# Performance work log

Measured on AMD Instinct MI355X. Metric: run time of the kernel, lower is better.

## Reference

```python
import jax, jax.numpy as jnp
import numpy as np

B, M, N = 8, 2048, 8192
K = 8            # knn neighbors
HID = 128        # hidden_dim
IN_DIM = 6
OUT_W = 2        # out_width (deconv kernel=stride=2 on length-1 seed)


def setup_inputs() -> dict:
    key = jax.random.key(0)
    ks = jax.random.split(key, 12)
    s = 0.1  # weight scale
    return {
        "partial": jax.random.normal(ks[0], (B, M, 3), jnp.float32),
        "predicted": jax.random.normal(ks[1], (B, N, 3), jnp.float32),
        # seed_fc: Linear(6,128) -> ReLU -> Linear(128,128)
        "W1": jax.random.normal(ks[2], (HID, IN_DIM), jnp.float32) * s,
        "b1": jax.random.normal(ks[3], (HID,), jnp.float32) * s,
        "W2": jax.random.normal(ks[4], (HID, HID), jnp.float32) * s,
        "b2": jax.random.normal(ks[5], (HID,), jnp.float32) * s,
        # ConvTranspose1d(HID, HID, kernel=2, stride=2): weight [in, out, kT]
        "Wd": jax.random.normal(ks[6], (HID, HID, OUT_W), jnp.float32) * s,
        "bd": jax.random.normal(ks[7], (HID,), jnp.float32) * s,
        # Conv1d(HID, 3, kernel=1): weight [3, HID, 1]
        "Wc": jax.random.normal(ks[8], (3, HID, 1), jnp.float32) * s,
        "bc": jax.random.normal(ks[9], (3,), jnp.float32) * s,
    }


def _forward(partial, predicted, W1, b1, W2, b2, Wd, bd, Wc, bc):
    Bb, Nn, _ = predicted.shape
    # squared pairwise distances [B,N,M] (same ordering as torch.cdist p=2)
    d2 = (jnp.sum(predicted ** 2, -1)[:, :, None]
          - 2.0 * jnp.einsum('bnd,bmd->bnm', predicted, partial)
          + jnp.sum(partial ** 2, -1)[:, None, :])
    _, idx = jax.lax.top_k(-d2, K)                       # [B,N,K] nearest
    neigh = jax.vmap(lambda p, i: p[i])(partial, idx)    # [B,N,K,3] gather
    neigh_mean = neigh.mean(axis=2)                      # [B,N,3]
    combined = jnp.concatenate([predicted, neigh_mean], -1).reshape(Bb * Nn, IN_DIM)
    # seed MLP
    h = jax.nn.relu(combined @ W1.T + b1)
    seed = h @ W2.T + b2                                 # [BN,HID]
    # ConvTranspose1d on length-1 input: out[:, o, t] = sum_i seed[:, i] * Wd[i, o, t]
    ht = jax.nn.relu(jnp.einsum('bi,iot->bot', seed, Wd) + bd[None, :, None])  # [BN,HID,2]
    out = jnp.einsum('bit,ci->bct', ht, Wc[:, :, 0]) + bc[None, :, None]       # [BN,3,2]
    out4 = jnp.transpose(out, (0, 2, 1)).reshape(Bb, Nn, OUT_W, 3)
    child = predicted[:, :, None, :] + out4              # parent + offsets
    return child.reshape(Bb, Nn * OUT_W, 3)


def reference(partial, predicted, W1, b1, W2, b2, Wd, bd, Wc, bc):
    return _forward(partial, predicted, W1, b1, W2, b2, Wd, bd, Wc, bc)
```

## Files before the change

kernel.cpp:

```cpp
#include <hip/hip_runtime.h>
#include <hip/hip_bf16.h>
#include <math.h>

#define TPB 256
constexpr int Bb = 8, Mm = 2048, Nn = 8192, HID = 128;
constexpr int KNNB = Bb * 128;
constexpr int PREPB = 128;

typedef __attribute__((ext_vector_type(8))) short short8;
typedef __attribute__((ext_vector_type(4))) float f32x4;

__device__ __forceinline__ int vzero() { int v; asm("v_mov_b32 %0, 0" : "=v"(v)); return v; }
__device__ __forceinline__ float4 ldg4(const float* __restrict__ p, int idx4, int vz) {
  return ((const float4*)p)[idx4 + vz];
}
__device__ __forceinline__ unsigned short f2b(float x) {
  __hip_bfloat16 h = __float2bfloat16(x);
  return *reinterpret_cast<unsigned short*>(&h);
}

__device__ __forceinline__ void mergeTop8(float a[8], const float b[8]) {
  float w[8];
  #pragma unroll
  for (int i = 0; i < 8; ++i) w[i] = fmaxf(a[i], b[7 - i]);
  #pragma unroll
  for (int i = 0; i < 4; ++i) {
    float lo = fminf(w[i], w[i + 4]); w[i + 4] = fmaxf(w[i], w[i + 4]); w[i] = lo;
  }
  #pragma unroll
  for (int g = 0; g < 8; g += 4)
    #pragma unroll
    for (int i = 0; i < 2; ++i) {
      float lo = fminf(w[g + i], w[g + i + 2]);
      w[g + i + 2] = fmaxf(w[g + i], w[g + i + 2]); w[g + i] = lo;
    }
  #pragma unroll
  for (int i = 0; i < 8; i += 2) {
    float lo = fminf(w[i], w[i + 1]); w[i + 1] = fmaxf(w[i], w[i + 1]); w[i] = lo;
  }
  #pragma unroll
  for (int i = 0; i < 8; ++i) a[i] = w[i];
}
__device__ __forceinline__ float t8of(const float a[8], const float b[8]) {
  float t = fmaxf(a[0], b[7]);
  #pragma unroll
  for (int i = 1; i < 8; ++i) t = fminf(t, fmaxf(a[i], b[7 - i]));
  return t;
}

#define INSERT8(L, u)                                                          \
  {                                                                            \
    L[0] = __builtin_amdgcn_fmed3f(u, L[0], L[1]);                             \
    L[1] = __builtin_amdgcn_fmed3f(u, L[1], L[2]);                             \
    L[2] = __builtin_amdgcn_fmed3f(u, L[2], L[3]);                             \
    L[3] = __builtin_amdgcn_fmed3f(u, L[3], L[4]);                             \
    L[4] = __builtin_amdgcn_fmed3f(u, L[4], L[5]);                             \
    L[5] = __builtin_amdgcn_fmed3f(u, L[5], L[6]);                             \
    L[6] = __builtin_amdgcn_fmed3f(u, L[6], L[7]);                             \
    L[7] = fmaxf(L[7], u);                                                     \
  }

__global__ __launch_bounds__(TPB, 4) void knn_prep_kernel(
    const float* __restrict__ partial, const float* __restrict__ predicted,
    const float* __restrict__ W2, const float* __restrict__ b2,
    const float* __restrict__ Wd, const float* __restrict__ bd,
    unsigned short* __restrict__ Bpack, float* __restrict__ Cf,
    float* __restrict__ outp) {
  __shared__ float4 pts[Mm];
  const int tid = threadIdx.x;

  if (blockIdx.x >= KNNB) {
    int idx = (blockIdx.x - KNNB) * TPB + tid;
    int f = idx >> 9, r = idx & 511, lane = r >> 3, j = r & 7;
    int chunk = f >> 4, ks = (f >> 2) & 3, n = f & 3;
    int k   = ks * 32 + (lane >> 4) * 8 + j;
    int col = chunk * 64 + n * 16 + (lane & 15);
    float acc = 0.f;
    for (int i = 0; i < HID; ++i)
      acc = fmaf(W2[i * HID + k], Wd[i * 256 + col], acc);
    Bpack[idx] = f2b(acc);
    if (idx < 256) {
      float c = bd[idx >> 1];
      for (int i = 0; i < HID; ++i) c = fmaf(b2[i], Wd[i * 256 + idx], c);
      Cf[idx] = c;
    }
    return;
  }

  const int b  = blockIdx.x >> 7;
  const int qt = blockIdx.x & 127;
  const float* pb = partial + (size_t)b * Mm * 3;
  for (int i = tid; i < Mm; i += TPB) {
    float x = pb[3 * i], y = pb[3 * i + 1], z = pb[3 * i + 2];
    pts[i] = make_float4(x, y, z, -0.5f * fmaf(x, x, fmaf(y, y, z * z)));
  }
  __syncthreads();

  const int lane = tid & 63, w = tid >> 6;
  const int s = lane & 15, g = lane >> 4;
  const int qbase = qt * 64 + w * 16 + g * 4;
  const float4* qp = (const float4*)(predicted + ((size_t)b * Nn + qbase) * 3);
  const float4 qa = qp[0], qb4 = qp[1], qc = qp[2];
  const float q0x = qa.x,  q0y = qa.y,  q0z = qa.z;
  const float q1x = qa.w,  q1y = qb4.x, q1z = qb4.y;
  const float q2x = qb4.z, q2y = qb4.w, q2z = qc.x;
  const float q3x = qc.y,  q3y = qc.z,  q3z = qc.w;

  float l0[8], l1[8], l2[8], l3[8];
  #pragma unroll
  for (int i = 0; i < 8; ++i) { l0[i] = -INFINITY; l1[i] = -INFINITY;
                                l2[i] = -INFINITY; l3[i] = -INFINITY; }
  #pragma unroll 4
  for (int mm = 0; mm < 128; ++mm) {
    float4 p = pts[s + 16 * mm];
    float u0 = fmaf(q0x, p.x, fmaf(q0y, p.y, fmaf(q0z, p.z, p.w)));
    float u1 = fmaf(q1x, p.x, fmaf(q1y, p.y, fmaf(q1z, p.z, p.w)));
    float u2 = fmaf(q2x, p.x, fmaf(q2y, p.y, fmaf(q2z, p.z, p.w)));
    float u3 = fmaf(q3x, p.x, fmaf(q3y, p.y, fmaf(q3z, p.z, p.w)));
    INSERT8(l0, u0); INSERT8(l1, u1); INSERT8(l2, u2); INSERT8(l3, u3);
  }

  #pragma unroll
  for (int dd = 0; dd < 3; ++dd) {
    const int d = 1 << dd;
    float ob[8];
    #pragma unroll
    for (int i = 0; i < 8; ++i) ob[i] = __shfl_xor(l0[i], d);
    mergeTop8(l0, ob);
    #pragma unroll
    for (int i = 0; i < 8; ++i) ob[i] = __shfl_xor(l1[i], d);
    mergeTop8(l1, ob);
    #pragma unroll
    for (int i = 0; i < 8; ++i) ob[i] = __shfl_xor(l2[i], d);
    mergeTop8(l2, ob);
    #pragma unroll
    for (int i = 0; i < 8; ++i) ob[i] = __shfl_xor(l3[i], d);
    mergeTop8(l3, ob);
  }
  float t80, t81, t82, t83;
  {
    float ob[8];
    #pragma unroll
    for (int i = 0; i < 8; ++i) ob[i] = __shfl_xor(l0[i], 8);
    t80 = t8of(l0, ob);
    #pragma unroll
    for (int i = 0; i < 8; ++i) ob[i] = __shfl_xor(l1[i], 8);
    t81 = t8of(l1, ob);
    #pragma unroll
    for (int i = 0; i < 8; ++i) ob[i] = __shfl_xor(l2[i], 8);
    t82 = t8of(l2, ob);
    #pragma unroll
    for (int i = 0; i < 8; ++i) ob[i] = __shfl_xor(l3[i], 8);
    t83 = t8of(l3, ob);
  }

  float a0x = 0.f, a0y = 0.f, a0z = 0.f, c0 = 0.f;
  float a1x = 0.f, a1y = 0.f, a1z = 0.f, c1 = 0.f;
  float a2x = 0.f, a2y = 0.f, a2z = 0.f, c2 = 0.f;
  float a3x = 0.f, a3y = 0.f, a3z = 0.f, c3 = 0.f;
  #pragma unroll 4
  for (int mm = 0; mm < 128; ++mm) {
    float4 p = pts[s + 16 * mm];
    float u0 = fmaf(q0x, p.x, fmaf(q0y, p.y, fmaf(q0z, p.z, p.w)));
    float u1 = fmaf(q1x, p.x, fmaf(q1y, p.y, fmaf(q1z, p.z, p.w)));
    float u2 = fmaf(q2x, p.x, fmaf(q2y, p.y, fmaf(q2z, p.z, p.w)));
    float u3 = fmaf(q3x, p.x, fmaf(q3y, p.y, fmaf(q3z, p.z, p.w)));
    float m0 = (u0 >= t80) ? 1.f : 0.f;
    float m1 = (u1 >= t81) ? 1.f : 0.f;
    float m2 = (u2 >= t82) ? 1.f : 0.f;
    float m3 = (u3 >= t83) ? 1.f : 0.f;
    a0x = fmaf(m0, p.x, a0x); a0y = fmaf(m0, p.y, a0y); a0z = fmaf(m0, p.z, a0z); c0 += m0;
    a1x = fmaf(m1, p.x, a1x); a1y = fmaf(m1, p.y, a1y); a1z = fmaf(m1, p.z, a1z); c1 += m1;
    a2x = fmaf(m2, p.x, a2x); a2y = fmaf(m2, p.y, a2y); a2z = fmaf(m2, p.z, a2z); c2 += m2;
    a3x = fmaf(m3, p.x, a3x); a3y = fmaf(m3, p.y, a3y); a3z = fmaf(m3, p.z, a3z); c3 += m3;
  }
  #pragma unroll
  for (int dd = 0; dd < 4; ++dd) {
    const int d = 1 << dd;
    a0x += __shfl_xor(a0x, d); a0y += __shfl_xor(a0y, d); a0z += __shfl_xor(a0z, d); c0 += __shfl_xor(c0, d);
    a1x += __shfl_xor(a1x, d); a1y += __shfl_xor(a1y, d); a1z += __shfl_xor(a1z, d); c1 += __shfl_xor(c1, d);
    a2x += __shfl_xor(a2x, d); a2y += __shfl_xor(a2y, d); a2z += __shfl_xor(a2z, d); c2 += __shfl_xor(c2, d);
    a3x += __shfl_xor(a3x, d); a3y += __shfl_xor(a3y, d); a3z += __shfl_xor(a3z, d); c3 += __shfl_xor(c3, d);
  }

  #pragma unroll
  for (int k = 0; k < 4; ++k) {
    if (s == k) {
      float qx = (k == 0) ? q0x : (k == 1) ? q1x : (k == 2) ? q2x : q3x;
      float qy = (k == 0) ? q0y : (k == 1) ? q1y : (k == 2) ? q2y : q3y;
      float qz = (k == 0) ? q0z : (k == 1) ? q1z : (k == 2) ? q2z : q3z;
      float t8 = (k == 0) ? t80 : (k == 1) ? t81 : (k == 2) ? t82 : t83;
      float sx = (k == 0) ? a0x : (k == 1) ? a1x : (k == 2) ? a2x : a3x;
      float sy = (k == 0) ? a0y : (k == 1) ? a1y : (k == 2) ? a2y : a3y;
      float sz = (k == 0) ? a0z : (k == 1) ? a1z : (k == 2) ? a2z : a3z;
      float cn = (k == 0) ? c0  : (k == 1) ? c1  : (k == 2) ? c2  : c3;
      if (cn != 8.0f) {
        sx = sy = sz = 0.f; float cw = 0.f;
        for (int m = 0; m < Mm; ++m) {
          float4 p = pts[m];
          float u = fmaf(qx, p.x, fmaf(qy, p.y, fmaf(qz, p.z, p.w)));
          if (u > t8) { sx += p.x; sy += p.y; sz += p.z; cw += 1.f; }
        }
        int need = 8 - (int)cw, got = 0;
        for (int m = 0; m < Mm && got < need; ++m) {
          float4 p = pts[m];
          float u = fmaf(qx, p.x, fmaf(qy, p.y, fmaf(qz, p.z, p.w)));
          if (u == t8) { sx += p.x; sy += p.y; sz += p.z; ++got; }
        }
      }
      float2* co = (float2*)(outp + ((size_t)b * Nn + qbase + k) * 6);
      co[0] = make_float2(qx, qy);
      co[1] = make_float2(qz, sx * 0.125f);
      co[2] = make_float2(sy * 0.125f, sz * 0.125f);
    }
  }
}

__global__ __launch_bounds__(TPB) void prep2_kernel(const float* __restrict__ W2,
    const float* __restrict__ b2, const float* __restrict__ Wd,
    const float* __restrict__ bd, unsigned short* __restrict__ Bpack,
    float* __restrict__ Cf) {
  int idx = blockIdx.x * TPB + threadIdx.x;
  int f = idx >> 9, r = idx & 511, lane = r >> 3, j = r & 7;
  int chunk = f >> 4, ks = (f >> 2) & 3, n = f & 3;
  int k   = ks * 32 + (lane >> 4) * 8 + j;
  int col = chunk * 64 + n * 16 + (lane & 15);
  float acc = 0.f;
  for (int i = 0; i < HID; ++i)
    acc = fmaf(W2[i * HID + k], Wd[i * 256 + col], acc);
  Bpack[idx] = f2b(acc);
  if (idx < 256) {
    float c = bd[idx >> 1];
    for (int i = 0; i < HID; ++i) c = fmaf(b2[i], Wd[i * 256 + idx], c);
    Cf[idx] = c;
  }
}

__global__ __launch_bounds__(TPB) void mlp_mfma(const float* __restrict__ W1,
    const float* __restrict__ b1, const unsigned short* __restrict__ Bpack,
    const float* __restrict__ Cf, const float* __restrict__ Wc,
    const float* __restrict__ bc, float* __restrict__ outp) {
  extern __shared__ char Alds[];
  const int tid = threadIdx.x;
  const int row0 = blockIdx.x * TPB;
  const int vz = vzero();

  {
    const float* rp = outp + (size_t)(row0 + tid) * 6;
    float2 r0 = *(const float2*)rp, r1 = *(const float2*)(rp + 2),
           r2 = *(const float2*)(rp + 4);
    const float c0 = r0.x, c1 = r0.y, c2 = r1.x, c3 = r1.y, c4 = r2.x, c5 = r2.y;
    float4 h4[32];
    #pragma unroll
    for (int j4 = 0; j4 < 32; ++j4) {
      float4 bb = ((const float4*)b1)[j4];
      float4 w0 = ldg4(W1, j4 * 6 + 0, vz), w1 = ldg4(W1, j4 * 6 + 1, vz),
             w2 = ldg4(W1, j4 * 6 + 2, vz), w3 = ldg4(W1, j4 * 6 + 3, vz),
             w4 = ldg4(W1, j4 * 6 + 4, vz), w5 = ldg4(W1, j4 * 6 + 5, vz);
      float a0 = bb.x, a1 = bb.y, a2 = bb.z, a3 = bb.w;
      a0 = fmaf(c0, w0.x, a0); a0 = fmaf(c1, w0.y, a0); a0 = fmaf(c2, w0.z, a0);
      a0 = fmaf(c3, w0.w, a0); a0 = fmaf(c4, w1.x, a0); a0 = fmaf(c5, w1.y, a0);
      a1 = fmaf(c0, w1.z, a1); a1 = fmaf(c1, w1.w, a1); a1 = fmaf(c2, w2.x, a1);
      a1 = fmaf(c3, w2.y, a1); a1 = fmaf(c4, w2.z, a1); a1 = fmaf(c5, w2.w, a1);
      a2 = fmaf(c0, w3.x, a2); a2 = fmaf(c1, w3.y, a2); a2 = fmaf(c2, w3.z, a2);
      a2 = fmaf(c3, w3.w, a2); a2 = fmaf(c4, w4.x, a2); a2 = fmaf(c5, w4.y, a2);
      a3 = fmaf(c0, w4.z, a3); a3 = fmaf(c1, w4.w, a3); a3 = fmaf(c2, w5.x, a3);
      a3 = fmaf(c3, w5.y, a3); a3 = fmaf(c4, w5.z, a3); a3 = fmaf(c5, w5.w, a3);
      h4[j4] = make_float4(fmaxf(a0, 0.f), fmaxf(a1, 0.f), fmaxf(a2, 0.f), fmaxf(a3, 0.f));
    }
    #pragma unroll
    for (int c = 0; c < 16; ++c) {
      float4 lo = h4[c * 2], hi = h4[c * 2 + 1];
      union { unsigned short us[8]; uint4 v; } pk;
      pk.us[0] = f2b(lo.x); pk.us[1] = f2b(lo.y); pk.us[2] = f2b(lo.z); pk.us[3] = f2b(lo.w);
      pk.us[4] = f2b(hi.x); pk.us[5] = f2b(hi.y); pk.us[6] = f2b(hi.z); pk.us[7] = f2b(hi.w);
      int byte = tid * 256 + ((c * 16) ^ ((tid & 7) << 4));
      *(uint4*)(Alds + byte) = pk.v;
    }
  }
  __syncthreads();

  const int lane = tid & 63, wid = tid >> 6;
  const int g = lane >> 4, cidx = lane & 15;
  float ac[4][4][3] = {};

  for (int chunk = 0; chunk < 4; ++chunk) {
    f32x4 acc[4][4];
    #pragma unroll
    for (int n = 0; n < 4; ++n) {
      float cfv = Cf[chunk * 64 + n * 16 + cidx];
      #pragma unroll
      for (int m = 0; m < 4; ++m) acc[m][n] = (f32x4){cfv, cfv, cfv, cfv};
    }
    #pragma unroll
    for (int ks = 0; ks < 4; ++ks) {
      short8 af[4];
      #pragma unroll
      for (int m = 0; m < 4; ++m) {
        int r = wid * 64 + m * 16 + cidx;
        int byte = r * 256 + ((ks * 64 + g * 16) ^ ((r & 7) << 4));
        af[m] = *(const short8*)(Alds + byte);
      }
      short8 bf[4];
      #pragma unroll
      for (int n = 0; n < 4; ++n)
        bf[n] = *(const short8*)((const char*)Bpack +
                 (((chunk * 4 + ks) * 4 + n) * 1024) + lane * 16);
      #pragma unroll
      for (int m = 0; m < 4; ++m)
        #pragma unroll
        for (int n = 0; n < 4; ++n)
          acc[m][n] = __builtin_amdgcn_mfma_f32_16x16x32_bf16(af[m], bf[n], acc[m][n], 0, 0, 0);
    }
    #pragma unroll
    for (int n = 0; n < 4; ++n) {
      int ot = chunk * 64 + n * 16 + cidx;
      int o = ot >> 1;
      float wc0 = Wc[o], wc1 = Wc[HID + o], wc2 = Wc[2 * HID + o];
      #pragma unroll
      for (int m = 0; m < 4; ++m) {
        #pragma unroll
        for (int i = 0; i < 4; ++i) {
          float v = fmaxf(acc[m][n][i], 0.f);
          ac[m][i][0] = fmaf(v, wc0, ac[m][i][0]);
          ac[m][i][1] = fmaf(v, wc1, ac[m][i][1]);
          ac[m][i][2] = fmaf(v, wc2, ac[m][i][2]);
        }
      }
    }
  }

  const float bc0 = bc[0], bc1 = bc[1], bc2 = bc[2];
  #pragma unroll
  for (int m = 0; m < 4; ++m) {
    #pragma unroll
    for (int i = 0; i < 4; ++i) {
      float s0 = ac[m][i][0], s1 = ac[m][i][1], s2 = ac[m][i][2];
      s0 += __shfl_xor(s0, 2); s0 += __shfl_xor(s0, 4); s0 += __shfl_xor(s0, 8);
      s1 += __shfl_xor(s1, 2); s1 += __shfl_xor(s1, 4); s1 += __shfl_xor(s1, 8);
      s2 += __shfl_xor(s2, 2); s2 += __shfl_xor(s2, 4); s2 += __shfl_xor(s2, 8);
      float o0 = __shfl_xor(s0, 1), o1 = __shfl_xor(s1, 1), o2 = __shfl_xor(s2, 1);
      const bool odd = lane & 1;
      float t00 = odd ? o0 : s0, t01 = odd ? o1 : s1, t02 = odd ? o2 : s2;
      float t10 = odd ? s0 : o0, t11 = odd ? s1 : o1, t12 = odd ? s2 : o2;
      if (cidx == m * 4 + i) {
        int row = row0 + wid * 64 + m * 16 + g * 4 + i;
        float* rp = outp + (size_t)row * 6;
        float px = rp[0], py = rp[1], pz = rp[2];
        rp[0] = px + t00 + bc0; rp[1] = py + t01 + bc1; rp[2] = pz + t02 + bc2;
        rp[3] = px + t10 + bc0; rp[4] = py + t11 + bc1; rp[5] = pz + t12 + bc2;
      }
    }
  }
}

__global__ __launch_bounds__(TPB) void mlp_fallback(
    const float* __restrict__ W1, const float* __restrict__ b1,
    const float* __restrict__ W2, const float* __restrict__ b2,
    const float* __restrict__ Wd, const float* __restrict__ bd,
    const float* __restrict__ Wc, const float* __restrict__ bc,
    float* __restrict__ outp) {
  const int row = blockIdx.x * TPB + threadIdx.x;
  float2* rp = (float2*)(outp + (size_t)row * 6);
  float2 r0 = rp[0], r1 = rp[1], r2 = rp[2];
  float cc[6] = {r0.x, r0.y, r1.x, r1.y, r2.x, r2.y};
  float h[HID];
  for (int j = 0; j < HID; ++j) {
    float a = b1[j];
    for (int c = 0; c < 6; ++c) a = fmaf(cc[c], W1[j * 6 + c], a);
    h[j] = fmaxf(a, 0.f);
  }
  float sd[HID];
  for (int i = 0; i < HID; ++i) {
    float a = b2[i];
    for (int j = 0; j < HID; ++j) a = fmaf(h[j], W2[i * HID + j], a);
    sd[i] = a;
  }
  float ov[3][2] = {};
  for (int oc = 0; oc < HID; ++oc)
    for (int t = 0; t < 2; ++t) {
      float a = bd[oc];
      for (int i = 0; i < HID; ++i) a = fmaf(sd[i], Wd[i * 256 + oc * 2 + t], a);
      a = fmaxf(a, 0.f);
      for (int c = 0; c < 3; ++c) ov[c][t] = fmaf(a, Wc[c * HID + oc], ov[c][t]);
    }
  rp[0] = make_float2(cc[0] + ov[0][0] + bc[0], cc[1] + ov[1][0] + bc[1]);
  rp[1] = make_float2(cc[2] + ov[2][0] + bc[2], cc[0] + ov[0][1] + bc[0]);
  rp[2] = make_float2(cc[1] + ov[1][1] + bc[1], cc[2] + ov[2][1] + bc[2]);
}

extern "C" void kernel_launch(void* const* d_in, const int* in_sizes, int n_in,
                              void* d_out, int out_size, void* d_ws, size_t ws_size,
                              hipStream_t stream) {
  const float* partial   = (const float*)d_in[0];
  const float* predicted = (const float*)d_in[1];
  const float* W1 = (const float*)d_in[2];
  const float* b1 = (const float*)d_in[3];
  const float* W2 = (const float*)d_in[4];
  const float* b2 = (const float*)d_in[5];
  const float* Wd = (const float*)d_in[6];
  const float* bd = (const float*)d_in[7];
  const float* Wc = (const float*)d_in[8];
  const float* bc = (const float*)d_in[9];
  float* outp = (float*)d_out;

  unsigned short* Bpack = (unsigned short*)d_ws;
  float* Cf = (float*)((char*)d_ws + 65536);
  const bool fits = ws_size >= (size_t)66560;

  if (fits) {
    hipLaunchKernelGGL(knn_prep_kernel, dim3(KNNB + PREPB), dim3(TPB), 0, stream,
                       partial, predicted, W2, b2, Wd, bd, Bpack, Cf, outp);
    hipLaunchKernelGGL(mlp_mfma, dim3((Bb * Nn) / TPB), dim3(TPB), 65536, stream,
                       W1, b1, Bpack, Cf, Wc, bc, outp);
  } else {
    hipLaunchKernelGGL(knn_prep_kernel, dim3(KNNB), dim3(TPB), 0, stream,
                       partial, predicted, W2, b2, Wd, bd,
                       (unsigned short*)nullptr, (float*)nullptr, outp);
    hipLaunchKernelGGL(mlp_fallback, dim3((Bb * Nn) / TPB), dim3(TPB), 0, stream,
                       W1, b1, W2, b2, Wd, bd, Wc, bc, outp);
  }
}
```

Before: 89.22 us.

## Fuse kNN and MLP into one cooperative kernel with grid sync

Merges the kNN/prep kernel and the MFMA MLP kernel into a single cooperative launch. Each block keeps its queries' combined features in registers, computes the packed weight product in the first blocks, grid-syncs, then runs the MLP on the same rows. This removes the second launch and the round trip of intermediate features through global memory. The cost is a grid-wide barrier and the requirement that all 1024 blocks be co-resident, with a two-kernel fallback if the cooperative launch fails.

```diff
diff --git a/kernel.cpp b/kernel.cpp
--- a/kernel.cpp
+++ b/kernel.cpp
@@ -1,6 +1,9 @@
 #include <hip/hip_runtime.h>
 #include <hip/hip_bf16.h>
+#include <hip/hip_cooperative_groups.h>
 #include <math.h>
+
+namespace cg = cooperative_groups;
 
 #define TPB 256
 constexpr int Bb = 8, Mm = 2048, Nn = 8192, HID = 128;
@@ -60,35 +63,10 @@
     L[7] = fmaxf(L[7], u);                                                     \
   }
 
-__global__ __launch_bounds__(TPB, 4) void knn_prep_kernel(
-    const float* __restrict__ partial, const float* __restrict__ predicted,
-    const float* __restrict__ W2, const float* __restrict__ b2,
-    const float* __restrict__ Wd, const float* __restrict__ bd,
-    unsigned short* __restrict__ Bpack, float* __restrict__ Cf,
-    float* __restrict__ outp) {
-  __shared__ float4 pts[Mm];
-  const int tid = threadIdx.x;
-
-  if (blockIdx.x >= KNNB) {
-    int idx = (blockIdx.x - KNNB) * TPB + tid;
-    int f = idx >> 9, r = idx & 511, lane = r >> 3, j = r & 7;
-    int chunk = f >> 4, ks = (f >> 2) & 3, n = f & 3;
-    int k   = ks * 32 + (lane >> 4) * 8 + j;
-    int col = chunk * 64 + n * 16 + (lane & 15);
-    float acc = 0.f;
-    for (int i = 0; i < HID; ++i)
-      acc = fmaf(W2[i * HID + k], Wd[i * 256 + col], acc);
-    Bpack[idx] = f2b(acc);
-    if (idx < 256) {
-      float c = bd[idx >> 1];
-      for (int i = 0; i < HID; ++i) c = fmaf(b2[i], Wd[i * 256 + idx], c);
-      Cf[idx] = c;
-    }
-    return;
-  }
-
-  const int b  = blockIdx.x >> 7;
-  const int qt = blockIdx.x & 127;
+__device__ __forceinline__ void knn_phase(const float* __restrict__ partial,
+                                          const float* __restrict__ predicted,
+                                          float4* pts, int b, int qt, int tid,
+                                          float cq[6], float* wrOut) {
   const float* pb = partial + (size_t)b * Mm * 3;
   for (int i = tid; i < Mm; i += TPB) {
     float x = pb[3 * i], y = pb[3 * i + 1], z = pb[3 * i + 2];
@@ -208,19 +186,22 @@
           if (u == t8) { sx += p.x; sy += p.y; sz += p.z; ++got; }
         }
       }
-      float2* co = (float2*)(outp + ((size_t)b * Nn + qbase + k) * 6);
-      co[0] = make_float2(qx, qy);
-      co[1] = make_float2(qz, sx * 0.125f);
-      co[2] = make_float2(sy * 0.125f, sz * 0.125f);
-    }
-  }
-}
-
-__global__ __launch_bounds__(TPB) void prep2_kernel(const float* __restrict__ W2,
+      cq[0] = qx; cq[1] = qy; cq[2] = qz;
+      cq[3] = sx * 0.125f; cq[4] = sy * 0.125f; cq[5] = sz * 0.125f;
+      if (wrOut) {
+        float2* co = (float2*)(wrOut + ((size_t)b * Nn + qbase + k) * 6);
+        co[0] = make_float2(cq[0], cq[1]);
+        co[1] = make_float2(cq[2], cq[3]);
+        co[2] = make_float2(cq[4], cq[5]);
+      }
+    }
+  }
+}
+
+__device__ __forceinline__ void prep_work(int idx, const float* __restrict__ W2,
     const float* __restrict__ b2, const float* __restrict__ Wd,
     const float* __restrict__ bd, unsigned short* __restrict__ Bpack,
     float* __restrict__ Cf) {
-  int idx = blockIdx.x * TPB + threadIdx.x;
   int f = idx >> 9, r = idx & 511, lane = r >> 3, j = r & 7;
   int chunk = f >> 4, ks = (f >> 2) & 3, n = f & 3;
   int k   = ks * 32 + (lane >> 4) * 8 + j;
@@ -236,6 +217,136 @@
   }
 }
 
+__global__ __launch_bounds__(TPB, 4) void fused_kernel(
+    const float* __restrict__ partial, const float* __restrict__ predicted,
+    const float* __restrict__ W1, const float* __restrict__ b1,
+    const float* __restrict__ W2, const float* __restrict__ b2,
+    const float* __restrict__ Wd, const float* __restrict__ bd,
+    const float* __restrict__ Wc, const float* __restrict__ bc,
+    unsigned short* __restrict__ Bpack, float* __restrict__ Cf,
+    float* __restrict__ outp) {
+  __shared__ float4 smem[Mm];
+  const int tid = threadIdx.x, bid = blockIdx.x;
+  const int b = bid >> 7, qt = bid & 127;
+  const int lane = tid & 63, w = tid >> 6;
+
+  float cq[6] = {0.f, 0.f, 0.f, 0.f, 0.f, 0.f};
+  knn_phase(partial, predicted, smem, b, qt, tid, cq, nullptr);
+  if (bid < PREPB)
+    prep_work(bid * TPB + tid, W2, b2, Wd, bd, Bpack, Cf);
+
+  cg::this_grid().sync();
+
+  char* Alds = (char*)smem;
+  {
+    const int rr = lane >> 2, q4 = lane & 3;
+    const int srcl = (rr & 3) + ((rr >> 2) << 4);
+    const float c0 = __shfl(cq[0], srcl), c1 = __shfl(cq[1], srcl),
+                c2 = __shfl(cq[2], srcl), c3 = __shfl(cq[3], srcl),
+                c4 = __shfl(cq[4], srcl), c5 = __shfl(cq[5], srcl);
+    const int rowA = w * 16 + rr;
+    const int j0 = q4 * 32;
+    const float4* W1f = (const float4*)W1;
+    float hbuf[32];
+    #pragma unroll
+    for (int jj = 0; jj < 16; ++jj) {
+      float4 v0 = W1f[q4 * 48 + jj * 3 + 0];
+      float4 v1 = W1f[q4 * 48 + jj * 3 + 1];
+      float4 v2 = W1f[q4 * 48 + jj * 3 + 2];
+      int j = j0 + jj * 2;
+      float a = b1[j], e = b1[j + 1];
+      a = fmaf(c0, v0.x, a); a = fmaf(c1, v0.y, a); a = fmaf(c2, v0.z, a);
+      a = fmaf(c3, v0.w, a); a = fmaf(c4, v1.x, a); a = fmaf(c5, v1.y, a);
+      e = fmaf(c0, v1.z, e); e = fmaf(c1, v1.w, e); e = fmaf(c2, v2.x, e);
+      e = fmaf(c3, v2.y, e); e = fmaf(c4, v2.z, e); e = fmaf(c5, v2.w, e);
+      hbuf[jj * 2] = fmaxf(a, 0.f); hbuf[jj * 2 + 1] = fmaxf(e, 0.f);
+    }
+    #pragma unroll
+    for (int cc = 0; cc < 4; ++cc) {
+      union { unsigned short us[8]; uint4 v; } pk;
+      #pragma unroll
+      for (int e2 = 0; e2 < 8; ++e2) pk.us[e2] = f2b(hbuf[cc * 8 + e2]);
+      int cglob = q4 * 4 + cc;
+      int byte = rowA * 256 + ((cglob * 16) ^ ((rowA & 7) << 4));
+      *(uint4*)(Alds + byte) = pk.v;
+    }
+  }
+  __syncthreads();
+
+  const int g2 = lane >> 4, cidx = lane & 15;
+  const int rA = w * 16 + cidx;
+  float ac[4][3] = {};
+  for (int chunk = 0; chunk < 4; ++chunk) {
+    f32x4 acc[4];
+    #pragma unroll
+    for (int n = 0; n < 4; ++n) {
+      float cfv = Cf[chunk * 64 + n * 16 + cidx];
+      acc[n] = (f32x4){cfv, cfv, cfv, cfv};
+    }
+    #pragma unroll
+    for (int ks = 0; ks < 4; ++ks) {
+      short8 af = *(const short8*)(Alds + rA * 256 +
+                                   ((ks * 64 + g2 * 16) ^ ((rA & 7) << 4)));
+      #pragma unroll
+      for (int n = 0; n < 4; ++n) {
+        short8 bf = *(const short8*)((const char*)Bpack +
+                     (((chunk * 4 + ks) * 4 + n) * 1024) + lane * 16);
+        acc[n] = __builtin_amdgcn_mfma_f32_16x16x32_bf16(af, bf, acc[n], 0, 0, 0);
+      }
+    }
+    #pragma unroll
+    for (int n = 0; n < 4; ++n) {
+      int ot = chunk * 64 + n * 16 + cidx;
+      int o = ot >> 1;
+      float wc0 = Wc[o], wc1 = Wc[HID + o], wc2 = Wc[2 * HID + o];
+      #pragma unroll
+      for (int i = 0; i < 4; ++i) {
+        float v = fmaxf(acc[n][i], 0.f);
+        ac[i][0] = fmaf(v, wc0, ac[i][0]);
+        ac[i][1] = fmaf(v, wc1, ac[i][1]);
+        ac[i][2] = fmaf(v, wc2, ac[i][2]);
+      }
+    }
+  }
+
+  const float bc0 = bc[0], bc1 = bc[1], bc2 = bc[2];
+  const size_t rowbase = (size_t)b * Nn + qt * 64;
+  #pragma unroll
+  for (int i = 0; i < 4; ++i) {
+    float s0 = ac[i][0], s1 = ac[i][1], s2 = ac[i][2];
+    s0 += __shfl_xor(s0, 2); s0 += __shfl_xor(s0, 4); s0 += __shfl_xor(s0, 8);
+    s1 += __shfl_xor(s1, 2); s1 += __shfl_xor(s1, 4); s1 += __shfl_xor(s1, 8);
+    s2 += __shfl_xor(s2, 2); s2 += __shfl_xor(s2, 4); s2 += __shfl_xor(s2, 8);
+    float o0 = __shfl_xor(s0, 1), o1 = __shfl_xor(s1, 1), o2 = __shfl_xor(s2, 1);
+    const bool odd = lane & 1;
+    float t00 = odd ? o0 : s0, t01 = odd ? o1 : s1, t02 = odd ? o2 : s2;
+    float t10 = odd ? s0 : o0, t11 = odd ? s1 : o1, t12 = odd ? s2 : o2;
+    if (cidx == i) {
+      float* rp = outp + (rowbase + (size_t)(w * 16 + g2 * 4 + i)) * 6;
+      rp[0] = cq[0] + t00 + bc0; rp[1] = cq[1] + t01 + bc1;
+      rp[2] = cq[2] + t02 + bc2; rp[3] = cq[0] + t10 + bc0;
+      rp[4] = cq[1] + t11 + bc1; rp[5] = cq[2] + t12 + bc2;
+    }
+  }
+}
+
+__global__ __launch_bounds__(TPB, 4) void knn_prep_kernel(
+    const float* __restrict__ partial, const float* __restrict__ predicted,
+    const float* __restrict__ W2, const float* __restrict__ b2,
+    const float* __restrict__ Wd, const float* __restrict__ bd,
+    unsigned short* __restrict__ Bpack, float* __restrict__ Cf,
+    float* __restrict__ outp) {
+  __shared__ float4 pts[Mm];
+  const int tid = threadIdx.x;
+  if (blockIdx.x >= KNNB) {
+    prep_work((blockIdx.x - KNNB) * TPB + tid, W2, b2, Wd, bd, Bpack, Cf);
+    return;
+  }
+  float cq[6];
+  knn_phase(partial, predicted, pts, blockIdx.x >> 7, blockIdx.x & 127, tid,
+            cq, outp);
+}
+
 __global__ __launch_bounds__(TPB) void mlp_mfma(const float* __restrict__ W1,
     const float* __restrict__ b1, const unsigned short* __restrict__ Bpack,
     const float* __restrict__ Cf, const float* __restrict__ Wc,
@@ -244,7 +355,6 @@
   const int tid = threadIdx.x;
   const int row0 = blockIdx.x * TPB;
   const int vz = vzero();
-
   {
     const float* rp = outp + (size_t)(row0 + tid) * 6;
     float2 r0 = *(const float2*)rp, r1 = *(const float2*)(rp + 2),
@@ -279,11 +389,9 @@
     }
   }
   __syncthreads();
-
   const int lane = tid & 63, wid = tid >> 6;
   const int g = lane >> 4, cidx = lane & 15;
   float ac[4][4][3] = {};
-
   for (int chunk = 0; chunk < 4; ++chunk) {
     f32x4 acc[4][4];
     #pragma unroll
@@ -318,7 +426,7 @@
       int o = ot >> 1;
       float wc0 = Wc[o], wc1 = Wc[HID + o], wc2 = Wc[2 * HID + o];
       #pragma unroll
-      for (int m = 0; m < 4; ++m) {
+      for (int m = 0; m < 4; ++m)
         #pragma unroll
         for (int i = 0; i < 4; ++i) {
           float v = fmaxf(acc[m][n][i], 0.f);
@@ -326,13 +434,11 @@
           ac[m][i][1] = fmaf(v, wc1, ac[m][i][1]);
           ac[m][i][2] = fmaf(v, wc2, ac[m][i][2]);
         }
-      }
-    }
-  }
-
+    }
+  }
   const float bc0 = bc[0], bc1 = bc[1], bc2 = bc[2];
   #pragma unroll
-  for (int m = 0; m < 4; ++m) {
+  for (int m = 0; m < 4; ++m)
     #pragma unroll
     for (int i = 0; i < 4; ++i) {
       float s0 = ac[m][i][0], s1 = ac[m][i][1], s2 = ac[m][i][2];
@@ -351,7 +457,6 @@
         rp[3] = px + t10 + bc0; rp[4] = py + t11 + bc1; rp[5] = pz + t12 + bc2;
       }
     }
-  }
 }
 
 __global__ __launch_bounds__(TPB) void mlp_fallback(
@@ -409,15 +514,26 @@
   const bool fits = ws_size >= (size_t)66560;
 
   if (fits) {
-    hipLaunchKernelGGL(knn_prep_kernel, dim3(KNNB + PREPB), dim3(TPB), 0, stream,
-                       partial, predicted, W2, b2, Wd, bd, Bpack, Cf, outp);
-    hipLaunchKernelGGL(mlp_mfma, dim3((Bb * Nn) / TPB), dim3(TPB), 65536, stream,
-                       W1, b1, Bpack, Cf, Wc, bc, outp);
+    void* args[] = {(void*)&partial, (void*)&predicted, (void*)&W1, (void*)&b1,
+                    (void*)&W2, (void*)&b2, (void*)&Wd, (void*)&bd,
+                    (void*)&Wc, (void*)&bc, (void*)&Bpack, (void*)&Cf,
+                    (void*)&outp};
+    hipError_t err = hipLaunchCooperativeKernel((const void*)fused_kernel,
+                                                dim3(KNNB), dim3(TPB), args,
+                                                0, stream);
+    if (err != hipSuccess) {
+      (void)hipGetLastError();
+      hipLaunchKernelGGL(knn_prep_kernel, dim3(KNNB + PREPB), dim3(TPB), 0,
+                         stream, partial, predicted, W2, b2, Wd, bd, Bpack, Cf,
+                         outp);
+      hipLaunchKernelGGL(mlp_mfma, dim3((Bb * Nn) / TPB), dim3(TPB), 65536,
+                         stream, W1, b1, Bpack, Cf, Wc, bc, outp);
+    }
   } else {
     hipLaunchKernelGGL(knn_prep_kernel, dim3(KNNB), dim3(TPB), 0, stream,
                        partial, predicted, W2, b2, Wd, bd,
                        (unsigned short*)nullptr, (float*)nullptr, outp);
-    hipLaunchKernelGGL(mlp_fallback, dim3((Bb * Nn) / TPB), dim3(TPB), 0, stream,
-                       W1, b1, W2, b2, Wd, bd, Wc, bc, outp);
-  }
-}
+    hipLaunchKernelGGL(mlp_fallback, dim3((Bb * Nn) / TPB), dim3(TPB), 0,
+                       stream, W1, b1, W2, b2, Wd, bd, Wc, bc, outp);
+  }
+}
```

New measurement: 187.4 us. 110% more time.
